# Optimization experiments

Hardware: AMD Instinct MI355X
Metric: run time of the kernel (lower is better)

## Reference

```python
import jax, jax.numpy as jnp
import numpy as np

N = 40000          # total samples; s pattern: first N//2 are group 0, rest group 1
TOP = 0.3          # top_percentile
LAM = 10.0
ITS = 10
P = 0.5


def setup_inputs() -> dict:
    key = jax.random.key(0)
    k1, k2 = jax.random.split(key)
    y_pred = jax.random.uniform(k1, (N,), dtype=jnp.float32)  # predicted probs in [0,1]
    # deterministic half/half sensitive attribute so group sizes are static
    s = (jnp.arange(N) >= N // 2).astype(jnp.int32)
    y_gt = jax.random.uniform(k2, (N,), dtype=jnp.float32)    # unused by forward math
    pct_a = jnp.full((1,), 0.2, dtype=jnp.float32)            # unused (threshold_based=False)
    pct_b = jnp.full((1,), 0.8, dtype=jnp.float32)            # unused
    return {"y_pred": y_pred, "s": s, "y_gt": y_gt, "pct_a": pct_a, "pct_b": pct_b}


def _wasserstein(y_pred):
    n = y_pred.shape[0]
    n0 = n // 2  # s==0 count (static: s is half zeros then half ones)
    y0 = y_pred[:n0]        # s == 0 group
    y1 = y_pred[n0:]        # s == 1 group
    nc = float(n0)
    nt = float(n - n0)
    # local_reg=True, threshold_based=False -> keep top `TOP` fraction after sort
    ia0 = int((1.0 - TOP) * n0)
    ia1 = int((1.0 - TOP) * (n - n0))
    y0 = jnp.sort(y0)[ia0:]  # (m0,)
    y1 = jnp.sort(y1)[ia1:]  # (m1,)
    m0 = y0.shape[0]
    m1 = y1.shape[0]
    # sqrt(cdist(.,p=2)**2) on 1-D points == |y1_i - y0_j|
    M = jnp.abs(y1[:, None] - y0[None, :])           # (m1, m0)
    delta = jax.lax.stop_gradient(jnp.max(M))
    eff_lam = jax.lax.stop_gradient(LAM / jnp.mean(M))
    # pad with slack row/col (delta cost, 0 in corner)
    row = delta * jnp.ones((1, m0), M.dtype)
    col = jnp.concatenate([delta * jnp.ones((m1, 1), M.dtype),
                           jnp.zeros((1, 1), M.dtype)], axis=0)
    Mt = jnp.concatenate([jnp.concatenate([M, row], axis=0), col], axis=1)  # (m1+1, m0+1)
    a = jnp.concatenate([P * jnp.ones((m1, 1), M.dtype) / nt,
                         (1.0 - P) * jnp.ones((1, 1), M.dtype)], axis=0)    # (m1+1, 1)
    b = jnp.concatenate([(1.0 - P) * jnp.ones((m0, 1), M.dtype) / nc,
                         P * jnp.ones((1, 1), M.dtype)], axis=0)            # (m0+1, 1)
    K = jnp.exp(-eff_lam * Mt) + 1e-6
    ainvK = K / a
    u = a
    for _ in range(ITS):  # fixed 10-step Sinkhorn fixed point
        u = 1.0 / (ainvK @ (b / (u.T @ K).T))
    v = b / (u.T @ K).T
    T = u * (v.T * K)
    T = jax.lax.stop_gradient(T)  # backpropT=False
    D = 2.0 * jnp.sum(T * Mt)
    return D


def reference(y_pred, s, y_gt, pct_a, pct_b):
    # s is the fixed half-zeros/half-ones pattern from setup_inputs; the static
    # slices in _wasserstein reproduce the original boolean masks exactly.
    reg_loss = _wasserstein(y_pred)
    z = jnp.zeros((1,), jnp.float32)
    return (reg_loss, z, z, z)
```

## Files before the change

### kernel.cpp

```cpp
#include <hip/hip_runtime.h>

#define HALF   20000
#define MSEL   6001
#define RANKLO 13999
#define CANDMAX 8192
#define THRESH 0.66f

#define NTHm  1024
#define TPTm  12
#define NWAVE 16
#define NTOT  12002
#define XPT   6
#define ESTR  13

#define OFF_CCNT  0
#define OFF_RANK  8
#define OFF_CANDV 16392
#define OFF_CANDI 32776

#define LXS  0
#define LYS  6144
#define LMV  12288
#define LEA  0
#define LEB  13312
#define LRED 26624
#define LSC  26688
#define SOLVE_LDS_FLOATS 26704
#define SOLVE_LDS_BYTES (SOLVE_LDS_FLOATS * 4)

__device__ __forceinline__ float fexp2(float x) {
#if defined(__has_builtin)
#if __has_builtin(__builtin_amdgcn_exp2f)
  return __builtin_amdgcn_exp2f(x);
#else
  return exp2f(x);
#endif
#else
  return exp2f(x);
#endif
}

__device__ __forceinline__ float frcp(float x) {
#if defined(__has_builtin)
#if __has_builtin(__builtin_amdgcn_rcpf)
  return __builtin_amdgcn_rcpf(x);
#else
  return 1.0f / x;
#endif
#else
  return 1.0f / x;
#endif
}

#if defined(__has_builtin)
#if __has_builtin(__builtin_amdgcn_update_dpp) && __has_builtin(__builtin_amdgcn_readlane)
#define HAS_DPP 1
#endif
#endif

#ifdef HAS_DPP
template<int CTRL, int RM>
__device__ __forceinline__ float dppadd(float x) {
  int s = __builtin_amdgcn_update_dpp(0, __float_as_int(x), CTRL, RM, 0xf, false);
  return x + __int_as_float(s);
}
__device__ __forceinline__ float prefix64(float x) {
  x = dppadd<0x111, 0xf>(x);
  x = dppadd<0x112, 0xf>(x);
  x = dppadd<0x114, 0xf>(x);
  x = dppadd<0x118, 0xf>(x);
  x = dppadd<0x142, 0xa>(x);
  x = dppadd<0x143, 0xc>(x);
  return x;
}
__device__ __forceinline__ float prefixrow(float x) {
  x = dppadd<0x111, 0xf>(x);
  x = dppadd<0x112, 0xf>(x);
  x = dppadd<0x114, 0xf>(x);
  x = dppadd<0x118, 0xf>(x);
  return x;
}
__device__ __forceinline__ float sufrow(float x) {
  x = dppadd<0x101, 0xf>(x);
  x = dppadd<0x102, 0xf>(x);
  x = dppadd<0x104, 0xf>(x);
  x = dppadd<0x108, 0xf>(x);
  return x;
}
__device__ __forceinline__ float rdlane(float x, int l) {
  return __int_as_float(__builtin_amdgcn_readlane(__float_as_int(x), l));
}
#else
__device__ __forceinline__ float prefix64(float x) {
  for (int d = 1; d < 64; d <<= 1) {
    float o = __shfl_up(x, d, 64);
    if ((threadIdx.x & 63) >= d) x += o;
  }
  return x;
}
__device__ __forceinline__ float prefixrow(float x) {
  for (int d = 1; d < 16; d <<= 1) {
    float o = __shfl_up(x, d, 64);
    if ((threadIdx.x & 15) >= d) x += o;
  }
  return x;
}
__device__ __forceinline__ float sufrow(float x) {
  for (int d = 1; d < 16; d <<= 1) {
    float o = __shfl_down(x, d, 64);
    if ((threadIdx.x & 15) + d < 16) x += o;
  }
  return x;
}
__device__ __forceinline__ float rdlane(float x, int l) { return __shfl(x, l, 64); }
#endif


__global__ __launch_bounds__(512) void k_cand(const float* __restrict__ yp, int* wsI, float* wsF) {
  __shared__ int woff[8];
  __shared__ int blkbase;
  const int h = blockIdx.y;
  const int tid = threadIdx.x;
  const int wv = tid >> 6, ln = tid & 63;
  const int idx = blockIdx.x * 512 + tid;
  float v = 0.f;
  bool flag = false;
  if (idx < HALF) {
    v = yp[h * HALF + idx];
    flag = (v >= THRESH);
  }
  unsigned long long mask = __ballot(flag);
  if (ln == 0) woff[wv] = __popcll(mask);
  __syncthreads();
  if (tid == 0) {
    int s = 0;
#pragma unroll
    for (int w = 0; w < 8; ++w) { int t = woff[w]; woff[w] = s; s += t; }
    blkbase = atomicAdd(&wsI[OFF_CCNT + h], s);
  }
  __syncthreads();
  if (flag) {
    int pos = blkbase + woff[wv] + (int)__popcll(mask & ((1ull << ln) - 1ull));
    if (pos < CANDMAX) {
      wsF[OFF_CANDV + h * CANDMAX + pos] = v;
      wsI[OFF_CANDI + h * CANDMAX + pos] = idx;
      wsI[OFF_RANK + h * CANDMAX + pos] = 0;
    }
  }
}

__global__ __launch_bounds__(512) void k_rankc(const int* __restrict__ wsIc, float* wsF, int* wsI) {
  __shared__ float cv[512];
  __shared__ int ci[512];
  const int h = blockIdx.z;
  const int tid = threadIdx.x;
  const int cnt = min(wsIc[OFF_CCNT + h], CANDMAX);
  const int cb = blockIdx.y * 512;
  if (cb >= cnt) return;
  const int clen = min(512, cnt - cb);
  if (tid < clen) {
    cv[tid] = wsF[OFF_CANDV + h * CANDMAX + cb + tid];
    ci[tid] = wsIc[OFF_CANDI + h * CANDMAX + cb + tid];
  }
  __syncthreads();
  const int g = blockIdx.x * 512 + tid;
  if (g >= cnt) return;
  const float v = wsF[OFF_CANDV + h * CANDMAX + g];
  const int li = wsIc[OFF_CANDI + h * CANDMAX + g];
  int r = 0;
  for (int l = 0; l < clen; ++l) {
    float w = cv[l];
    r += (w < v || (w == v && ci[l] < li)) ? 1 : 0;
  }
  atomicAdd(&wsI[OFF_RANK + h * CANDMAX + g], r);
}


__device__ __forceinline__ float block_reduce(float v, float* red) {
  const int tid = threadIdx.x;
  __syncthreads();
  for (int d = 1; d < 64; d <<= 1) v += __shfl_xor(v, d, 64);
  if ((tid & 63) == 0) red[tid >> 6] = v;
  __syncthreads();
  float r = 0.f;
  if (tid < NWAVE) {
    r = red[tid];
    for (int d = 1; d < NWAVE; d <<= 1) r += __shfl_xor(r, d, 64);
    if (tid == 0) red[0] = r;
  }
  __syncthreads();
  return red[0];
}

__device__ __forceinline__ int bsearch_leq(const float* arr, float v) {
  int lo = 0, hi = MSEL;
  while (lo < hi) {
    int m = (lo + hi) >> 1;
    if (arr[m] <= v) lo = m + 1; else hi = m;
  }
  return lo;
}
__device__ __forceinline__ int bsearch_lt(const float* arr, float v) {
  int lo = 0, hi = MSEL;
  while (lo < hi) {
    int m = (lo + hi) >> 1;
    if (arr[m] < v) lo = m + 1; else hi = m;
  }
  return lo;
}

template<bool DO_W>
__device__ __forceinline__ void scan_core(float (&a)[TPTm], float (&b)[TPTm], float wsum,
                                          float* lds, float& GA, float& GB,
                                          int sout, int lout, float lnext) {
  float* red = lds + LRED;
  float* scal = lds + LSC;
  const int tid = threadIdx.x;
  const int wv = tid >> 6, ln = tid & 63;
  float ta = 0.f;
#pragma unroll
  for (int k = 0; k < TPTm; ++k) { float t = a[k]; a[k] = ta; ta += t; }
  float tb = 0.f;
#pragma unroll
  for (int k = TPTm - 1; k >= 0; --k) { tb += b[k]; b[k] = tb; }

  float tsA = __shfl_up(ta, 1, 64);
  if (ln == 0) tsA = 0.f;
  const float eA = prefix64(tsA);
  const float wTotA = rdlane(eA, 63) + rdlane(ta, 63);

  float tsB = __shfl_down(tb, 1, 64);
  if (ln == 63) tsB = 0.f;
  const float sRow = sufrow(tsB);
  const float r1 = rdlane(sRow, 16);
  const float r2 = rdlane(sRow, 32);
  const float r3 = rdlane(sRow, 48);
  const int row = ln >> 4;
  const float radd = (row == 0) ? (r1 + r2 + r3)
                   : (row == 1) ? (r2 + r3)
                   : (row == 2) ? r3 : 0.f;
  const float eB = sRow + radd;
  const float wTotB = rdlane(eB, 0) + rdlane(tb, 0);

  float wTotW = 0.f;
  if (DO_W) {
    float iW = prefix64(wsum);
    wTotW = rdlane(iW, 63);
  }
  if (ln == 0) {
    red[wv] = wTotA;
    red[16 + wv] = wTotB;
    if (DO_W) red[32 + wv] = wTotW;
  }
  __syncthreads();
  float tAs = (ln >= 1 && ln < NWAVE) ? red[ln - 1] : 0.f;
  const float pAe = prefixrow(tAs);
  const float GAoff = rdlane(pAe, wv);
  float tBr = (ln < NWAVE) ? red[16 + (NWAVE - 1 - ln)] : 0.f;
  const float pBr = prefixrow(tBr);
  const float GBoff = (wv < NWAVE - 1) ? rdlane(pBr, (NWAVE - 2) - wv) : 0.f;
  if (tid == 0) {
    red[48] = rdlane(pAe, NWAVE - 1) + red[NWAVE - 1];
    red[49] = rdlane(pBr, NWAVE - 1);
    if (DO_W) {
      float s = 0.f;
#pragma unroll
      for (int q = 0; q < NWAVE; ++q) s += red[32 + q];
      scal[sout] = s;
      scal[lout] = lnext;
    }
  }
  GA = GAoff + eA;
  GB = GBoff + eB;
  __syncthreads();
}

template<int MODE, int SRCY>
__device__ __forceinline__ void mpass(float* lds, float (&z)[TPTm],
                                      unsigned vmask, unsigned ymask,
                                      int sin, int lin, int sout, int lout) {
  float* scal = lds + LSC;
  const float* EAl = lds + LEA + threadIdx.x * ESTR;
  const float* EBl = lds + LEB + threadIdx.x * ESTR;
  const float au = 0.5f / 20000.0f;
  float cin = 0.f, lnext = 0.f;
  if (MODE) {
    const float kd = scal[2];
    float S_in, l_in;
    if (MODE == 1) { S_in = (float)MSEL * au; l_in = 0.5f; }
    else { S_in = scal[sin]; l_in = scal[lin]; }
    cin = 1e-6f * S_in + l_in * kd;
    lnext = 0.5f * frcp(kd * S_in + l_in * (1.0f + 1e-6f));
  }
  float a[TPTm], b[TPTm];
  float wsum = 0.f;
#pragma unroll
  for (int k = 0; k < TPTm; ++k) {
    bool isy = (ymask >> k) & 1u;
    bool val = (vmask >> k) & 1u;
    bool src = val && (isy == (SRCY != 0));
    float w = src ? (MODE ? au * frcp(z[k] + cin) : au) : 0.f;
    wsum += w;
    a[k] = w * EAl[k];
    b[k] = w * EBl[k];
  }
  float GA, GB;
  scan_core<(MODE != 0)>(a, b, wsum, lds, GA, GB, sout, lout, lnext);
#pragma unroll
  for (int k = 0; k < TPTm; ++k) {
    bool isy = (ymask >> k) & 1u;
    bool val = (vmask >> k) & 1u;
    if (val && (isy != (SRCY != 0)))
      z[k] = EBl[k] * (GA + a[k]) + EAl[k] * (GB + b[k]);
  }
}

__global__ __launch_bounds__(NTHm) void k_solve(const float* __restrict__ wsF,
                                                const int* __restrict__ wsI,
                                                float* __restrict__ out) {
  extern __shared__ float lds[];
  const int tid = threadIdx.x;
  float* xs = lds + LXS;
  float* ys = lds + LYS;
  float* mv = lds + LMV;
  float* red = lds + LRED;
  float* scal = lds + LSC;
  const float au = 0.5f / 20000.0f;
  const int base = tid * TPTm;

#pragma unroll
  for (int k = 0; k < XPT; ++k) {
    xs[tid * XPT + k] = 1e30f;
    ys[tid * XPT + k] = 1e30f;
  }
#pragma unroll
  for (int k = 0; k < TPTm; ++k) mv[base + k] = 1e30f;
  __syncthreads();

  for (int h = 0; h < 2; ++h) {
    const int cnt = min(wsI[OFF_CCNT + h], CANDMAX);
    float* dst = h ? ys : xs;
    for (int c = tid; c < cnt; c += NTHm) {
      int full = wsI[OFF_RANK + h * CANDMAX + c] + (HALF - cnt);
      if (full >= RANKLO) dst[full - RANKLO] = wsF[OFF_CANDV + h * CANDMAX + c];
    }
  }
  __syncthreads();

  {
    const int i0 = tid * XPT;
    if (i0 < MSEL) {
      int p = 0;
#pragma unroll
      for (int k = 0; k < XPT; ++k) {
        int i = i0 + k;
        if (i >= MSEL) break;
        float x = xs[i];
        if (k == 0) p = bsearch_leq(ys, x);
        else { while (ys[p] <= x) ++p; }
        mv[i + p] = x;
      }
      int q = 0;
#pragma unroll
      for (int k = 0; k < XPT; ++k) {
        int j = i0 + k;
        if (j >= MSEL) break;
        float y = ys[j];
        if (k == 0) q = bsearch_lt(xs, y);
        else { while (xs[q] < y) ++q; }
        mv[j + q] = -y;
      }
    }
  }
  __syncthreads();

  float vv[TPTm], z[TPTm];
  unsigned vmask = 0, ymask = 0;
#pragma unroll
  for (int k = 0; k < TPTm; ++k) {
    int g = base + k;
    float m = mv[g];
    bool val = (g < NTOT);
    bool isy = (m < 0.f);
    vv[k] = val ? fabsf(m) : 0.f;
    if (val) vmask |= (1u << k);
    if (val && isy) ymask |= (1u << k);
    z[k] = 0.f;
  }
  float bx0 = 0.f, bxl = 0.f, by0 = 0.f, byl = 0.f;
  if (tid == 0) {
    bx0 = xs[0]; bxl = xs[MSEL - 1];
    by0 = ys[0]; byl = ys[MSEL - 1];
  }

  {
    float a[TPTm], b[TPTm];
#pragma unroll
    for (int k = 0; k < TPTm; ++k) {
      bool isy = (ymask >> k) & 1u;
      a[k] = isy ? vv[k] : 0.f;
      b[k] = isy ? 1.f : 0.f;
    }
    float GA, GB;
    scan_core<false>(a, b, 0.f, lds, GA, GB, 0, 0, 0.f);
    const float PyT = red[48];
    float rs = 0.f;
#pragma unroll
    for (int k = 0; k < TPTm; ++k) {
      bool val = (vmask >> k) & 1u;
      bool isy = (ymask >> k) & 1u;
      if (val && !isy) {
        float P = GA + a[k];
        float S = GB + b[k];
        float p = (float)MSEL - S;
        rs += vv[k] * (2.f * p - (float)MSEL) + PyT - 2.f * P;
      }
    }
    float tot = block_reduce(rs, red);
    if (tid == 0) {
      float meanM = tot / ((float)MSEL * (float)MSEL);
      float lam = 10.0f / meanM;
      float lamL2 = lam * 1.4426950408889634f;
      float delta = fmaxf(byl - bx0, bxl - by0);
      float kd = fexp2(-lamL2 * delta) + 1e-6f;
      float lo = fminf(bx0, by0);
      float hi = fmaxf(bxl, byl);
      scal[0] = lamL2;
      scal[1] = delta;
      scal[2] = kd;
      scal[3] = 0.5f * (lo + hi);
    }
  }
  __syncthreads();

  {
    const float lamL2 = scal[0];
    const float mid = scal[3];
    float* EAw = lds + LEA + tid * ESTR;
    float* EBw = lds + LEB + tid * ESTR;
#pragma unroll
    for (int k = 0; k < TPTm; ++k) {
      float e1 = 0.f, e2 = 0.f;
      if ((vmask >> k) & 1u) {
        float X = lamL2 * (vv[k] - mid);
        e1 = fexp2(X);
        e2 = fexp2(-X);
      }
      EAw[k] = e1;
      EBw[k] = e2;
    }
  }
  __syncthreads();

  mpass<0, 1>(lds, z, vmask, ymask, 0, 0, 0, 0);
  mpass<1, 0>(lds, z, vmask, ymask, 5, 7, 4, 6);
  mpass<2, 1>(lds, z, vmask, ymask, 4, 6, 5, 7);
  for (int it = 1; it < 10; ++it) {
    mpass<2, 0>(lds, z, vmask, ymask, 5, 7, 4, 6);
    mpass<2, 1>(lds, z, vmask, ymask, 4, 6, 5, 7);
  }

  const float delta = scal[1], kd2 = scal[2];
  const float Sx = scal[4], Sy = scal[5], lX = scal[6], lY = scal[7];
  const float cin_v = 1e-6f * Sy + lY * kd2;
  const float cin_u = 1e-6f * Sx + lX * kd2;
  const float* EAl = lds + LEA + tid * ESTR;
  const float* EBl = lds + LEB + tid * ESTR;

  float dv[TPTm];
  float a[TPTm], b[TPTm];
  float GA, GB;
#pragma unroll
  for (int k = 0; k < TPTm; ++k) {
    bool isx = ((vmask >> k) & 1u) && !((ymask >> k) & 1u);
    float vw = isx ? au * frcp(z[k] + cin_v) : 0.f;
    a[k] = vw * EAl[k];
    b[k] = vw * EBl[k];
  }
  scan_core<false>(a, b, 0.f, lds, GA, GB, 0, 0, 0.f);
#pragma unroll
  for (int k = 0; k < TPTm; ++k) {
    dv[k] = ((ymask >> k) & 1u)
          ? vv[k] * (EBl[k] * (GA + a[k]) - EAl[k] * (GB + b[k])) : 0.f;
  }
#pragma unroll
  for (int k = 0; k < TPTm; ++k) {
    bool isx = ((vmask >> k) & 1u) && !((ymask >> k) & 1u);
    float vwx = isx ? (au * frcp(z[k] + cin_v)) * vv[k] : 0.f;
    a[k] = vwx * EAl[k];
    b[k] = vwx * EBl[k];
  }
  scan_core<false>(a, b, 0.f, lds, GA, GB, 0, 0, 0.f);
#pragma unroll
  for (int k = 0; k < TPTm; ++k) {
    if ((ymask >> k) & 1u)
      dv[k] += -EBl[k] * (GA + a[k]) + EAl[k] * (GB + b[k]);
  }
#pragma unroll
  for (int k = 0; k < TPTm; ++k) {
    bool isx = ((vmask >> k) & 1u) && !((ymask >> k) & 1u);
    float vw = isx ? au * frcp(z[k] + cin_v) : 0.f;
    a[k] = vw;
    b[k] = vw * vv[k];
  }
  scan_core<false>(a, b, 0.f, lds, GA, GB, 0, 0, 0.f);
  const float Sv = red[48];
  const float TVX = red[49];
  float acc = 0.f;
#pragma unroll
  for (int k = 0; k < TPTm; ++k) {
    if ((ymask >> k) & 1u) {
      float P = GA + a[k];
      float S = GB + b[k];
      float d6 = dv[k] + 1e-6f * (vv[k] * (2.f * P - Sv) + 2.f * S - TVX);
      float u = au * frcp(z[k] + cin_u);
      acc += u * d6;
    }
  }
  float Dc = block_reduce(acc, red);
  if (tid == 0) {
    float v_last = 0.5f / (kd2 * Sy + lY * (1.0f + 1e-6f));
    float D = Dc + delta * kd2 * (lY * Sv + v_last * Sy);
    out[0] = 2.0f * D;
    out[1] = 0.f;
    out[2] = 0.f;
    out[3] = 0.f;
  }
}

extern "C" void kernel_launch(void* const* d_in, const int* in_sizes, int n_in,
                              void* d_out, int out_size, void* d_ws, size_t ws_size,
                              hipStream_t stream) {
  const float* yp = (const float*)d_in[0];
  float* wsF = (float*)d_ws;
  int* wsI = (int*)d_ws;
  float* out = (float*)d_out;

  hipMemsetAsync((char*)d_ws + OFF_CCNT * 4, 0, 8, stream);
  k_cand<<<dim3(40, 2), 512, 0, stream>>>(yp, wsI, wsF);
  k_rankc<<<dim3(16, 16, 2), 512, 0, stream>>>(wsI, wsF, wsI);
  k_solve<<<1, NTHm, SOLVE_LDS_BYTES, stream>>>(wsF, wsI, out);
}
```

Measured before the change: 106.2 us.

## Double-buffer scan reduction slots and drop second barrier, derive exp(-x) via rcp

Each scan now alternates between two LDS reduction banks, so the trailing __syncthreads per scan can be removed. Totals are computed redundantly by every thread through wave shuffles instead of being broadcast by thread 0 through LDS. The second exponential table (exp(-X)) is dropped and replaced by a reciprocal of the first, which halves the table's LDS footprint and traffic but adds rcp work per element. Invalid entries are now set to 1 instead of 0. For large |X| the reciprocal of exp2 may under- or overflow differently from computing exp2(-X) directly.

```diff
diff --git a/kernel.cpp b/kernel.cpp
--- a/kernel.cpp
+++ b/kernel.cpp
@@ -22,10 +22,9 @@
 #define LYS  6144
 #define LMV  12288
 #define LEA  0
-#define LEB  13312
-#define LRED 26624
-#define LSC  26688
-#define SOLVE_LDS_FLOATS 26704
+#define LRED 24576
+#define LSC  24704
+#define SOLVE_LDS_FLOATS 24720
 #define SOLVE_LDS_BYTES (SOLVE_LDS_FLOATS * 4)
 
 __device__ __forceinline__ float fexp2(float x) {
@@ -211,10 +210,9 @@
 
 template<bool DO_W>
 __device__ __forceinline__ void scan_core(float (&a)[TPTm], float (&b)[TPTm], float wsum,
-                                          float* lds, float& GA, float& GB,
-                                          int sout, int lout, float lnext) {
-  float* red = lds + LRED;
-  float* scal = lds + LSC;
+                                          float* lds, int bank, float& GA, float& GB,
+                                          float& totA, float& totB, float& totW) {
+  float* red = lds + LRED + bank;
   const int tid = threadIdx.x;
   const int wv = tid >> 6, ln = tid & 63;
   float ta = 0.f;
@@ -256,39 +254,30 @@
   float tAs = (ln >= 1 && ln < NWAVE) ? red[ln - 1] : 0.f;
   const float pAe = prefixrow(tAs);
   const float GAoff = rdlane(pAe, wv);
+  totA = rdlane(pAe, NWAVE - 1) + red[NWAVE - 1];
   float tBr = (ln < NWAVE) ? red[16 + (NWAVE - 1 - ln)] : 0.f;
   const float pBr = prefixrow(tBr);
   const float GBoff = (wv < NWAVE - 1) ? rdlane(pBr, (NWAVE - 2) - wv) : 0.f;
-  if (tid == 0) {
-    red[48] = rdlane(pAe, NWAVE - 1) + red[NWAVE - 1];
-    red[49] = rdlane(pBr, NWAVE - 1);
-    if (DO_W) {
-      float s = 0.f;
-#pragma unroll
-      for (int q = 0; q < NWAVE; ++q) s += red[32 + q];
-      scal[sout] = s;
-      scal[lout] = lnext;
-    }
+  totB = rdlane(pBr, NWAVE - 1);
+  if (DO_W) {
+    float tW = (ln < NWAVE) ? red[32 + ln] : 0.f;
+    float pW = prefixrow(tW);
+    totW = rdlane(pW, NWAVE - 1);
   }
   GA = GAoff + eA;
   GB = GBoff + eB;
-  __syncthreads();
 }
 
 template<int MODE, int SRCY>
-__device__ __forceinline__ void mpass(float* lds, float (&z)[TPTm],
-                                      unsigned vmask, unsigned ymask,
-                                      int sin, int lin, int sout, int lout) {
-  float* scal = lds + LSC;
+__device__ __forceinline__ void mpass(float* lds, int bank, float (&z)[TPTm],
+                                      unsigned vmask, unsigned ymask, float kd,
+                                      float S_in, float l_in,
+                                      float& S_out, float& l_out) {
   const float* EAl = lds + LEA + threadIdx.x * ESTR;
-  const float* EBl = lds + LEB + threadIdx.x * ESTR;
   const float au = 0.5f / 20000.0f;
   float cin = 0.f, lnext = 0.f;
   if (MODE) {
-    const float kd = scal[2];
-    float S_in, l_in;
     if (MODE == 1) { S_in = (float)MSEL * au; l_in = 0.5f; }
-    else { S_in = scal[sin]; l_in = scal[lin]; }
     cin = 1e-6f * S_in + l_in * kd;
     lnext = 0.5f * frcp(kd * S_in + l_in * (1.0f + 1e-6f));
   }
@@ -301,18 +290,22 @@
     bool src = val && (isy == (SRCY != 0));
     float w = src ? (MODE ? au * frcp(z[k] + cin) : au) : 0.f;
     wsum += w;
-    a[k] = w * EAl[k];
-    b[k] = w * EBl[k];
-  }
-  float GA, GB;
-  scan_core<(MODE != 0)>(a, b, wsum, lds, GA, GB, sout, lout, lnext);
+    float ea = EAl[k];
+    a[k] = w * ea;
+    b[k] = w * frcp(ea);
+  }
+  float GA, GB, tA, tB, tW;
+  scan_core<(MODE != 0)>(a, b, wsum, lds, bank, GA, GB, tA, tB, tW);
 #pragma unroll
   for (int k = 0; k < TPTm; ++k) {
     bool isy = (ymask >> k) & 1u;
     bool val = (vmask >> k) & 1u;
-    if (val && (isy != (SRCY != 0)))
-      z[k] = EBl[k] * (GA + a[k]) + EAl[k] * (GB + b[k]);
-  }
+    if (val && (isy != (SRCY != 0))) {
+      float ea = EAl[k];
+      z[k] = frcp(ea) * (GA + a[k]) + ea * (GB + b[k]);
+    }
+  }
+  if (MODE) { S_out = tW; l_out = lnext; }
 }
 
 __global__ __launch_bounds__(NTHm) void k_solve(const float* __restrict__ wsF,
@@ -401,9 +394,8 @@
       a[k] = isy ? vv[k] : 0.f;
       b[k] = isy ? 1.f : 0.f;
     }
-    float GA, GB;
-    scan_core<false>(a, b, 0.f, lds, GA, GB, 0, 0, 0.f);
-    const float PyT = red[48];
+    float GA, GB, PyT, tB, tW;
+    scan_core<false>(a, b, 0.f, lds, 0, GA, GB, PyT, tB, tW);
     float rs = 0.f;
 #pragma unroll
     for (int k = 0; k < TPTm; ++k) {
@@ -433,68 +425,69 @@
   }
   __syncthreads();
 
+  const float lamL2 = scal[0];
+  const float delta = scal[1];
+  const float kd = scal[2];
+  const float mid = scal[3];
   {
-    const float lamL2 = scal[0];
-    const float mid = scal[3];
     float* EAw = lds + LEA + tid * ESTR;
-    float* EBw = lds + LEB + tid * ESTR;
 #pragma unroll
     for (int k = 0; k < TPTm; ++k) {
-      float e1 = 0.f, e2 = 0.f;
-      if ((vmask >> k) & 1u) {
-        float X = lamL2 * (vv[k] - mid);
-        e1 = fexp2(X);
-        e2 = fexp2(-X);
-      }
+      float e1 = 1.0f;
+      if ((vmask >> k) & 1u) e1 = fexp2(lamL2 * (vv[k] - mid));
       EAw[k] = e1;
-      EBw[k] = e2;
-    }
-  }
-  __syncthreads();
-
-  mpass<0, 1>(lds, z, vmask, ymask, 0, 0, 0, 0);
-  mpass<1, 0>(lds, z, vmask, ymask, 5, 7, 4, 6);
-  mpass<2, 1>(lds, z, vmask, ymask, 4, 6, 5, 7);
+    }
+  }
+  __syncthreads();
+
+  float Sx = 0.f, lX = 0.f, Sy = 0.f, lY = 0.f;
+  int bk = 48;
+  mpass<0, 1>(lds, bk, z, vmask, ymask, kd, 0.f, 0.f, Sx, lX); bk ^= 48;
+  mpass<1, 0>(lds, bk, z, vmask, ymask, kd, 0.f, 0.f, Sx, lX); bk ^= 48;
+  mpass<2, 1>(lds, bk, z, vmask, ymask, kd, Sx, lX, Sy, lY); bk ^= 48;
   for (int it = 1; it < 10; ++it) {
-    mpass<2, 0>(lds, z, vmask, ymask, 5, 7, 4, 6);
-    mpass<2, 1>(lds, z, vmask, ymask, 4, 6, 5, 7);
-  }
-
-  const float delta = scal[1], kd2 = scal[2];
-  const float Sx = scal[4], Sy = scal[5], lX = scal[6], lY = scal[7];
-  const float cin_v = 1e-6f * Sy + lY * kd2;
-  const float cin_u = 1e-6f * Sx + lX * kd2;
+    mpass<2, 0>(lds, bk, z, vmask, ymask, kd, Sy, lY, Sx, lX); bk ^= 48;
+    mpass<2, 1>(lds, bk, z, vmask, ymask, kd, Sx, lX, Sy, lY); bk ^= 48;
+  }
+
+  const float cin_v = 1e-6f * Sy + lY * kd;
+  const float cin_u = 1e-6f * Sx + lX * kd;
   const float* EAl = lds + LEA + tid * ESTR;
-  const float* EBl = lds + LEB + tid * ESTR;
 
   float dv[TPTm];
   float a[TPTm], b[TPTm];
-  float GA, GB;
+  float GA, GB, tA, tB, tW;
 #pragma unroll
   for (int k = 0; k < TPTm; ++k) {
     bool isx = ((vmask >> k) & 1u) && !((ymask >> k) & 1u);
     float vw = isx ? au * frcp(z[k] + cin_v) : 0.f;
-    a[k] = vw * EAl[k];
-    b[k] = vw * EBl[k];
-  }
-  scan_core<false>(a, b, 0.f, lds, GA, GB, 0, 0, 0.f);
-#pragma unroll
-  for (int k = 0; k < TPTm; ++k) {
-    dv[k] = ((ymask >> k) & 1u)
-          ? vv[k] * (EBl[k] * (GA + a[k]) - EAl[k] * (GB + b[k])) : 0.f;
+    float ea = EAl[k];
+    a[k] = vw * ea;
+    b[k] = vw * frcp(ea);
+  }
+  scan_core<false>(a, b, 0.f, lds, bk, GA, GB, tA, tB, tW); bk ^= 48;
+#pragma unroll
+  for (int k = 0; k < TPTm; ++k) {
+    if ((ymask >> k) & 1u) {
+      float ea = EAl[k];
+      dv[k] = vv[k] * (frcp(ea) * (GA + a[k]) - ea * (GB + b[k]));
+    } else dv[k] = 0.f;
   }
 #pragma unroll
   for (int k = 0; k < TPTm; ++k) {
     bool isx = ((vmask >> k) & 1u) && !((ymask >> k) & 1u);
     float vwx = isx ? (au * frcp(z[k] + cin_v)) * vv[k] : 0.f;
-    a[k] = vwx * EAl[k];
-    b[k] = vwx * EBl[k];
-  }
-  scan_core<false>(a, b, 0.f, lds, GA, GB, 0, 0, 0.f);
-#pragma unroll
-  for (int k = 0; k < TPTm; ++k) {
-    if ((ymask >> k) & 1u)
-      dv[k] += -EBl[k] * (GA + a[k]) + EAl[k] * (GB + b[k]);
+    float ea = EAl[k];
+    a[k] = vwx * ea;
+    b[k] = vwx * frcp(ea);
+  }
+  scan_core<false>(a, b, 0.f, lds, bk, GA, GB, tA, tB, tW); bk ^= 48;
+#pragma unroll
+  for (int k = 0; k < TPTm; ++k) {
+    if ((ymask >> k) & 1u) {
+      float ea = EAl[k];
+      dv[k] += -frcp(ea) * (GA + a[k]) + ea * (GB + b[k]);
+    }
   }
 #pragma unroll
   for (int k = 0; k < TPTm; ++k) {
@@ -503,9 +496,9 @@
     a[k] = vw;
     b[k] = vw * vv[k];
   }
-  scan_core<false>(a, b, 0.f, lds, GA, GB, 0, 0, 0.f);
-  const float Sv = red[48];
-  const float TVX = red[49];
+  scan_core<false>(a, b, 0.f, lds, bk, GA, GB, tA, tB, tW);
+  const float Sv = tA;
+  const float TVX = tB;
   float acc = 0.f;
 #pragma unroll
   for (int k = 0; k < TPTm; ++k) {
@@ -519,8 +512,8 @@
   }
   float Dc = block_reduce(acc, red);
   if (tid == 0) {
-    float v_last = 0.5f / (kd2 * Sy + lY * (1.0f + 1e-6f));
-    float D = Dc + delta * kd2 * (lY * Sv + v_last * Sy);
+    float v_last = 0.5f / (kd * Sy + lY * (1.0f + 1e-6f));
+    float D = Dc + delta * kd * (lY * Sv + v_last * Sy);
     out[0] = 2.0f * D;
     out[1] = 0.f;
     out[2] = 0.f;
```

After: 104.6 us. Within noise of the previous version (-1.5%).
